# Performance work log

Measured on AMD Instinct MI355X. Metric: run time of the kernel, lower is better.

The kernel has to match this reference:

```python
import jax, jax.numpy as jnp
import numpy as np

REG_MAX = 16
BOX_W = 7.5
OBJ_W = 1.0
TOPK = 10
EPS = 1e-7


def dfl_decode(x, reg_max):
    # x: [B, 4*reg_max, N] -> expected value of per-side distribution -> [B, N, 4] (xyxy)
    B, C, N = x.shape
    x = x.reshape(B, 4, reg_max, N)
    p = jax.nn.softmax(x, axis=2)
    proj = jnp.arange(reg_max, dtype=x.dtype)
    return jnp.einsum('bkrn,r->bnk', p, proj)


def bbox_ciou(b1, b2):
    # b1: [B,N,1,4], b2: [B,1,M,4], xyxy -> [B,N,M]
    x11, y11, x12, y12 = b1[..., 0], b1[..., 1], b1[..., 2], b1[..., 3]
    x21, y21, x22, y22 = b2[..., 0], b2[..., 1], b2[..., 2], b2[..., 3]
    w1, h1 = x12 - x11, y12 - y11
    w2, h2 = x22 - x21, y22 - y21
    iw = jnp.clip(jnp.minimum(x12, x22) - jnp.maximum(x11, x21), 0.0)
    ih = jnp.clip(jnp.minimum(y12, y22) - jnp.maximum(y11, y21), 0.0)
    inter = iw * ih
    union = w1 * h1 + w2 * h2 - inter + EPS
    iou = inter / union
    cw = jnp.maximum(x12, x22) - jnp.minimum(x11, x21)
    ch = jnp.maximum(y12, y22) - jnp.minimum(y11, y21)
    c2 = cw * cw + ch * ch + EPS
    rho2 = ((x21 + x22 - x11 - x12) ** 2 + (y21 + y22 - y11 - y12) ** 2) * 0.25
    v = (4.0 / (np.pi ** 2)) * (jnp.arctan(w2 / (h2 + EPS)) - jnp.arctan(w1 / (h1 + EPS))) ** 2
    alpha = jax.lax.stop_gradient(v / (v - iou + 1.0 + EPS))
    return iou - rho2 / c2 - alpha * v


def setup_inputs() -> dict:
    key = jax.random.key(0)
    k1, k2, k3, k4 = jax.random.split(key, 4)
    B, N, M = 8, 34000, 64
    boxes = jax.random.normal(k1, (B, 4 * REG_MAX, N), dtype=jnp.float32)
    scores = jax.random.normal(k2, (B, N), dtype=jnp.float32)
    # GT boxes: valid xyxy in roughly the same [0, reg_max) range as decoded preds
    xy = jax.random.uniform(k3, (B, M, 2), dtype=jnp.float32) * 11.0
    wh = jax.random.uniform(k4, (B, M, 2), dtype=jnp.float32) * 4.0 + 0.5
    targets = jnp.concatenate([xy, xy + wh], axis=-1)
    return {'boxes': boxes, 'scores': scores, 'targets': targets}


def reference(boxes, scores, targets):
    B, N = scores.shape
    M = targets.shape[1]
    pb = dfl_decode(boxes, REG_MAX)                     # [B,N,4]
    ciou = bbox_ciou(pb[:, :, None, :], targets[:, None, :, :])  # [B,N,M]
    k = min(TOPK, N)
    topv, topi = jax.lax.top_k(jnp.swapaxes(ciou, 1, 2), k)      # [B,M,k] over anchors
    valid = topv > 0.0
    vals = jnp.where(valid, topv, 0.0)

    def per_batch(idx, val, vld):
        flat_i = idx.reshape(-1)
        iou_t = jnp.zeros((N,), val.dtype).at[flat_i].max(val.reshape(-1))
        pos = jnp.zeros((N,), bool).at[flat_i].max(vld.reshape(-1))
        return iou_t, pos

    iou_target, pos = jax.vmap(per_batch)(topi, vals, valid)     # [B,N]
    posf = pos.astype(iou_target.dtype)
    npos = posf.sum(axis=1)
    box_per = jnp.where(npos > 0,
                        ((1.0 - iou_target) * posf).sum(axis=1) / jnp.maximum(npos, 1.0),
                        0.0)
    box_loss = box_per.sum()
    # BCEWithLogits (mean over anchors), summed over batch
    bce = jnp.maximum(scores, 0.0) - scores * iou_target + jnp.log1p(jnp.exp(-jnp.abs(scores)))
    obj_loss = bce.mean(axis=1).sum()
    total = (BOX_W * box_loss + OBJ_W * obj_loss) / B
    return total, box_loss, obj_loss
```

## Files before the change

### kernel.cpp

```cpp
#include <hip/hip_runtime.h>
#include <math.h>

#define BQ 8
#define MQ 64
#define KTOP 10
#define EPSQ 1e-7f
#define APB 256
#define MBUF 1344

__device__ __forceinline__ float frcp(float x) { return __builtin_amdgcn_rcpf(x); }

#define EV16(G, OUT)                                                           \
  {                                                                            \
    float mx = fmaxf(fmaxf(fmaxf(fmaxf(G##0, G##1), fmaxf(G##2, G##3)),        \
                           fmaxf(fmaxf(G##4, G##5), fmaxf(G##6, G##7))),       \
                     fmaxf(fmaxf(fmaxf(G##8, G##9), fmaxf(G##10, G##11)),      \
                           fmaxf(fmaxf(G##12, G##13), fmaxf(G##14, G##15))));  \
    float s = 0.f, ws = 0.f, e;                                                \
    e = __expf(G##0 - mx); s += e;                                             \
    e = __expf(G##1 - mx); s += e; ws += 1.f * e;                              \
    e = __expf(G##2 - mx); s += e; ws += 2.f * e;                              \
    e = __expf(G##3 - mx); s += e; ws += 3.f * e;                              \
    e = __expf(G##4 - mx); s += e; ws += 4.f * e;                              \
    e = __expf(G##5 - mx); s += e; ws += 5.f * e;                              \
    e = __expf(G##6 - mx); s += e; ws += 6.f * e;                              \
    e = __expf(G##7 - mx); s += e; ws += 7.f * e;                              \
    e = __expf(G##8 - mx); s += e; ws += 8.f * e;                              \
    e = __expf(G##9 - mx); s += e; ws += 9.f * e;                              \
    e = __expf(G##10 - mx); s += e; ws += 10.f * e;                            \
    e = __expf(G##11 - mx); s += e; ws += 11.f * e;                            \
    e = __expf(G##12 - mx); s += e; ws += 12.f * e;                            \
    e = __expf(G##13 - mx); s += e; ws += 13.f * e;                            \
    e = __expf(G##14 - mx); s += e; ws += 14.f * e;                            \
    e = __expf(G##15 - mx); s += e; ws += 15.f * e;                            \
    OUT = ws * frcp(s);                                                        \
  }

#define DECL_LDS16(RB, G)                                                      \
  float G##0 = tile[(RB) + 0][tid], G##1 = tile[(RB) + 1][tid],                \
        G##2 = tile[(RB) + 2][tid], G##3 = tile[(RB) + 3][tid],                \
        G##4 = tile[(RB) + 4][tid], G##5 = tile[(RB) + 5][tid],                \
        G##6 = tile[(RB) + 6][tid], G##7 = tile[(RB) + 7][tid],                \
        G##8 = tile[(RB) + 8][tid], G##9 = tile[(RB) + 9][tid],                \
        G##10 = tile[(RB) + 10][tid], G##11 = tile[(RB) + 11][tid],            \
        G##12 = tile[(RB) + 12][tid], G##13 = tile[(RB) + 13][tid],            \
        G##14 = tile[(RB) + 14][tid], G##15 = tile[(RB) + 15][tid];

__global__ __launch_bounds__(256) void decode_topk_kernel(
    const float* __restrict__ boxes, const float* __restrict__ scores,
    const float* __restrict__ targets, unsigned int* __restrict__ iou_bits,
    uint2* __restrict__ cand, float* __restrict__ bcePartial,
    unsigned int* __restrict__ ctr, int N, int bpb) {
  const int tid = threadIdx.x;
  const int b = blockIdx.x / bpb;
  const int blk = blockIdx.x - b * bpb;
  const int a0 = blk * APB;
  const int w = tid >> 6;
  const int l = tid & 63;

  __shared__ __align__(16) char u_raw[32 * APB * sizeof(float)];
  float(*tile)[APB] = (float(*)[APB])u_raw;
  float* s_hv = (float*)u_raw;
  int* s_hi = (int*)(u_raw + 4 * MQ * KTOP * 4);
  uint2* s_mg = (uint2*)(u_raw + 8 * MQ * KTOP * 4);

  __shared__ float4 s_sv[APB];
  __shared__ float s_at[APB];
  __shared__ int s_ix[APB];
  __shared__ int s_cnt;
  __shared__ float s_bce;
  if (tid == 0) { s_cnt = 0; s_bce = 0.f; }
  if (blockIdx.x == 0 && tid == 0) *ctr = 0u;
  __syncthreads();

  const size_t Ns = (size_t)N;

  const int n = a0 + tid;
  float bce0 = 0.f;
  if (n < N) {
    const size_t i = (size_t)b * N + n;
    iou_bits[i] = 0u;
    float sc = scores[i];
    bce0 = fmaxf(sc, 0.f) + log1pf(__expf(-fabsf(sc)));
  }

  auto stage32 = [&](int row0) {
    const float* gbase = boxes + (size_t)(b * 64 + row0) * Ns + a0;
    if (a0 + APB <= N) {
#pragma unroll
      for (int k = 0; k < 8; ++k) {
        int idx = tid + (k << 8);
        int r = idx >> 6;
        int c = (idx & 63) << 2;
        *(float4*)&tile[r][c] = *(const float4*)(gbase + (size_t)r * Ns + c);
      }
    } else {
      int rem = N - a0;
#pragma unroll
      for (int k = 0; k < 8; ++k) {
        int idx = tid + (k << 8);
        int r = idx >> 6;
        int c = (idx & 63) << 2;
        for (int j = 0; j < 4; ++j)
          tile[r][c + j] = (c + j < rem) ? gbase[(size_t)r * Ns + c + j] : 0.f;
      }
    }
  };

  float e0, e1, e2, e3;
  stage32(0);
  __syncthreads();
  { DECL_LDS16(0, A) EV16(A, e0) }
  { DECL_LDS16(16, Bv) EV16(Bv, e1) }
  __syncthreads();
  stage32(32);
  __syncthreads();
  { DECL_LDS16(0, Cv) EV16(Cv, e2) }
  { DECL_LDS16(16, Dv) EV16(Dv, e3) }

  bool pred = false;
  float at = 0.f;
  if (n < N) {
    float w1 = e2 - e0, h1 = e3 - e1;
    if (w1 > 0.f && h1 > 0.f) {
      pred = true;
      at = atanf(w1 * frcp(h1 + EPSQ));
    }
  }
  {
    unsigned long long mask = __ballot(pred);
    int cnt = __popcll(mask);
    int bslot = 0;
    if (l == 0 && cnt) bslot = atomicAdd(&s_cnt, cnt);
    bslot = __shfl(bslot, 0, 64);
    if (pred) {
      int pos = bslot + __popcll(mask & ((1ull << l) - 1ull));
      s_sv[pos] = make_float4(e0, e1, e2, e3);
      s_at[pos] = at;
      s_ix[pos] = n;
    }
  }
#pragma unroll
  for (int d = 1; d < 64; d <<= 1) bce0 += __shfl_xor(bce0, d, 64);
  if (l == 0) atomicAdd(&s_bce, bce0);
  __syncthreads();
  const int nsurv = s_cnt;
  if (tid == 0) bcePartial[blockIdx.x] = s_bce;

  const float4 t = ((const float4*)targets)[b * MQ + l];
  const float x21 = t.x, y21 = t.y, x22 = t.z, y22 = t.w;
  const float w2 = x22 - x21, h2 = y22 - y21;
  const float atan_t = atanf(w2 * frcp(h2 + EPSQ));
  const float area2 = w2 * h2, sumx2 = x21 + x22, sumy2 = y21 + y22;
  const float CPI = 4.0f / (float)(M_PI * M_PI);

  float hv0 = 0.f, hv1 = 0.f, hv2 = 0.f, hv3 = 0.f, hv4 = 0.f;
  float hv5 = 0.f, hv6 = 0.f, hv7 = 0.f, hv8 = 0.f, hv9 = 0.f;
  int hi0 = 0, hi1 = 0, hi2 = 0, hi3 = 0, hi4 = 0;
  int hi5 = 0, hi6 = 0, hi7 = 0, hi8 = 0, hi9 = 0;

  const int qlen = (nsurv + 3) >> 2;
  const int j0 = w * qlen;
  const int j1 = min(nsurv, j0 + qlen);
  for (int j = j0; j < j1; ++j) {
    float4 p = s_sv[j];
    float pa = s_at[j];
    int ixj = s_ix[j];
    float x11 = p.x, y11 = p.y, x12 = p.z, y12 = p.w;
    float w1 = x12 - x11, h1 = y12 - y11;
    float iw = fmaxf(fminf(x12, x22) - fmaxf(x11, x21), 0.f);
    float ih = fmaxf(fminf(y12, y22) - fmaxf(y11, y21), 0.f);
    float inter = iw * ih;
    float uni = w1 * h1 + area2 - inter + EPSQ;
    float iou = inter * frcp(uni);
    float cw = fmaxf(x12, x22) - fminf(x11, x21);
    float ch = fmaxf(y12, y22) - fminf(y11, y21);
    float c2 = cw * cw + ch * ch + EPSQ;
    float dx = sumx2 - x11 - x12;
    float dy = sumy2 - y11 - y12;
    float rho2 = (dx * dx + dy * dy) * 0.25f;
    float da = atan_t - pa;
    float v = CPI * da * da;
    float alpha = v * frcp(v - iou + 1.f + EPSQ);
    float ciou = iou - rho2 * frcp(c2) - alpha * v;
    if (ciou > hv9) {
      float cv = ciou;
      int ci = ixj;
#define INS(vk, ik)                         \
  {                                         \
    bool gt = cv > vk;                      \
    float tv_ = vk; int ti_ = ik;           \
    vk = gt ? cv : vk; ik = gt ? ci : ik;   \
    cv = gt ? tv_ : cv; ci = gt ? ti_ : ci; \
  }
      INS(hv0, hi0) INS(hv1, hi1) INS(hv2, hi2) INS(hv3, hi3) INS(hv4, hi4)
      INS(hv5, hi5) INS(hv6, hi6) INS(hv7, hi7) INS(hv8, hi8) INS(hv9, hi9)
#undef INS
    }
  }
  const int hb = (w * MQ + l) * KTOP;
  s_hv[hb + 0] = hv0; s_hi[hb + 0] = hi0;
  s_hv[hb + 1] = hv1; s_hi[hb + 1] = hi1;
  s_hv[hb + 2] = hv2; s_hi[hb + 2] = hi2;
  s_hv[hb + 3] = hv3; s_hi[hb + 3] = hi3;
  s_hv[hb + 4] = hv4; s_hi[hb + 4] = hi4;
  s_hv[hb + 5] = hv5; s_hi[hb + 5] = hi5;
  s_hv[hb + 6] = hv6; s_hi[hb + 6] = hi6;
  s_hv[hb + 7] = hv7; s_hi[hb + 7] = hi7;
  s_hv[hb + 8] = hv8; s_hi[hb + 8] = hi8;
  s_hv[hb + 9] = hv9; s_hi[hb + 9] = hi9;
  __syncthreads();

  if (w == 0) {
    const int m = l;
    int p0 = 0, p1 = 0, p2 = 0, p3 = 0;
    for (int r = 0; r < KTOP; ++r) {
      float c0 = s_hv[(0 * MQ + m) * KTOP + p0];
      float c1 = s_hv[(1 * MQ + m) * KTOP + p1];
      float c2m = s_hv[(2 * MQ + m) * KTOP + p2];
      float c3 = s_hv[(3 * MQ + m) * KTOP + p3];
      float best = c0; int bw = 0;
      if (c1 > best) { best = c1; bw = 1; }
      if (c2m > best) { best = c2m; bw = 2; }
      if (c3 > best) { best = c3; bw = 3; }
      int psel = (bw == 0) ? p0 : (bw == 1) ? p1 : (bw == 2) ? p2 : p3;
      int bidx = s_hi[(bw * MQ + m) * KTOP + psel];
      s_mg[m * KTOP + r] = make_uint2(__float_as_uint(best), (unsigned)bidx);
      if (bw == 0) p0 = min(p0 + 1, KTOP - 1);
      else if (bw == 1) p1 = min(p1 + 1, KTOP - 1);
      else if (bw == 2) p2 = min(p2 + 1, KTOP - 1);
      else p3 = min(p3 + 1, KTOP - 1);
    }
  }
  __syncthreads();
  uint2* obase = cand + (size_t)(b * bpb + blk) * (MQ * KTOP);
  for (int sl = tid; sl < MQ * KTOP; sl += 256) obase[sl] = s_mg[sl];
}

__device__ __forceinline__ void select_top10(
    float* s_bv, int* s_bi, float* s_winv, int* s_wini,
    int* s_cnt, int c, int tid) {
  if (tid < 64) {
    for (int r = 0; r < KTOP; ++r) {
      float bv = 0.f;
      int bs = 0xffff;
      for (int sl = tid; sl < c; sl += 64) {
        float v = s_bv[sl];
        if (v > bv) { bv = v; bs = sl; }
      }
      unsigned long long key =
          ((unsigned long long)__float_as_uint(bv) << 32) | (unsigned int)bs;
#pragma unroll
      for (int d = 1; d < 64; d <<= 1) {
        unsigned long long o = __shfl_xor(key, d, 64);
        if (o > key) key = o;
      }
      if (tid == 0) {
        float wv = __uint_as_float((unsigned int)(key >> 32));
        int ws = (int)(key & 0xffffu);
        s_winv[r] = wv;
        if (wv > 0.f && ws != 0xffff) {
          s_wini[r] = s_bi[ws];
          s_bv[ws] = 0.f;
        } else {
          s_wini[r] = 0;
        }
      }
    }
    if (tid < KTOP) { s_bv[tid] = s_winv[tid]; s_bi[tid] = s_wini[tid]; }
    if (tid == 0) *s_cnt = KTOP;
  }
}

__global__ __launch_bounds__(256) void merge_kernel(
    const uint2* __restrict__ cand, const float* __restrict__ scores,
    unsigned int* __restrict__ iou_bits, const float* __restrict__ bcePartial,
    float* __restrict__ mergePartial, unsigned int* __restrict__ ctr,
    float* __restrict__ out, int N, int bpb) {
  const int bm = blockIdx.x;
  const int b = bm >> 6;
  const int m = bm & 63;
  const int tid = threadIdx.x;
  const int l = tid & 63;
  const int NC = bpb * KTOP;

  __shared__ float s_bv[MBUF];
  __shared__ int s_bi[MBUF];
  __shared__ float s_winv[KTOP];
  __shared__ int s_wini[KTOP];
  __shared__ int s_cnt;
  __shared__ float s_d[3];
  __shared__ int s_last;
  __shared__ float s_acc[BQ * 3];
  if (tid == 0) s_cnt = 0;
  if (tid < 3) s_d[tid] = 0.f;
  if (tid < BQ * 3) s_acc[tid] = 0.f;
  __syncthreads();

  for (int k2 = tid; k2 < NC; k2 += 256) {
    int blkk = k2 / KTOP;
    int r = k2 - blkk * KTOP;
    uint2 e = cand[((size_t)(b * bpb + blkk) * MQ + m) * KTOP + r];
    float v = __uint_as_float(e.x);
    bool p = v > 0.f;
    unsigned long long mask = __ballot(p);
    int cnt = __popcll(mask);
    int bslot = 0;
    if (l == 0 && cnt) bslot = atomicAdd(&s_cnt, cnt);
    bslot = __shfl(bslot, 0, 64);
    if (p) {
      int pos = bslot + __popcll(mask & ((1ull << l) - 1ull));
      s_bv[pos] = v;
      s_bi[pos] = (int)e.y;
    }
  }
  __syncthreads();
  int c = s_cnt;
  __syncthreads();
  if (c > KTOP) {
    select_top10(s_bv, s_bi, s_winv, s_wini, &s_cnt, c, tid);
    __syncthreads();
    c = KTOP;
  }
  if (tid < KTOP && tid < c) {
    float v = s_bv[tid];
    if (v > 0.f) {
      int ix = s_bi[tid];
      unsigned int vb = __float_as_uint(v);
      unsigned int old = atomicMax(&iou_bits[(size_t)b * N + ix], vb);
      if (old < vb) {
        float vold = __uint_as_float(old);
        bool was = (old != 0u);
        atomicAdd(&s_d[0], was ? (vold - v) : (1.f - v));
        if (!was) atomicAdd(&s_d[1], 1.f);
        atomicAdd(&s_d[2], -scores[(size_t)b * N + ix] * (v - vold));
      }
    }
  }
  __syncthreads();
  if (tid == 0) {
    float4* mp = (float4*)(mergePartial + (size_t)bm * 4);
    *mp = make_float4(s_d[0], s_d[1], s_d[2], 0.f);
    __threadfence();
    unsigned int done = atomicAdd(ctr, 1u);
    s_last = (done == (unsigned)(gridDim.x - 1)) ? 1 : 0;
  }
  __syncthreads();
  if (s_last) {
    __threadfence();
    volatile const float* mp = mergePartial;
    for (int i = tid; i < BQ * MQ; i += 256) {
      int bb = i >> 6;
      float a0 = mp[i * 4 + 0];
      float a1 = mp[i * 4 + 1];
      float a2 = mp[i * 4 + 2];
      atomicAdd(&s_acc[bb * 3 + 0], a0);
      atomicAdd(&s_acc[bb * 3 + 1], a1);
      atomicAdd(&s_acc[bb * 3 + 2], a2);
    }
    volatile const float* bp = bcePartial;
    for (int i = tid; i < BQ * bpb; i += 256) {
      int bb = i / bpb;
      atomicAdd(&s_acc[bb * 3 + 2], bp[i]);
    }
    __syncthreads();
    if (tid == 0) {
      float box = 0.f, obj = 0.f;
      for (int bb = 0; bb < BQ; ++bb) {
        float np = s_acc[bb * 3 + 1];
        box += (np > 0.f) ? s_acc[bb * 3 + 0] / fmaxf(np, 1.f) : 0.f;
        obj += s_acc[bb * 3 + 2] / (float)N;
      }
      out[0] = (7.5f * box + obj) / (float)BQ;
      out[1] = box;
      out[2] = obj;
    }
  }
}

extern "C" void kernel_launch(void* const* d_in, const int* in_sizes, int n_in,
                              void* d_out, int out_size, void* d_ws, size_t ws_size,
                              hipStream_t stream) {
  const float* boxes = (const float*)d_in[0];
  const float* scores = (const float*)d_in[1];
  const float* targets = (const float*)d_in[2];
  float* out = (float*)d_out;
  const int N = in_sizes[1] / BQ;

  const int bpb = (N + APB - 1) / APB;
  const int nblk = BQ * bpb;

  char* ws = (char*)d_ws;
  size_t cand_bytes = (size_t)BQ * bpb * MQ * KTOP * sizeof(uint2);
  size_t iou_bytes = (size_t)BQ * N * sizeof(unsigned int);
  size_t bce_bytes = (((size_t)nblk * sizeof(float)) + 255) & ~(size_t)255;
  size_t mp_bytes = (size_t)BQ * MQ * 4 * sizeof(float);

  uint2* cand = (uint2*)ws;                    ws += cand_bytes;
  unsigned int* iou_bits = (unsigned int*)ws;  ws += iou_bytes;
  float* bcePartial = (float*)ws;              ws += bce_bytes;
  float* mergePartial = (float*)ws;            ws += mp_bytes;
  unsigned int* ctr = (unsigned int*)ws;

  decode_topk_kernel<<<nblk, 256, 0, stream>>>(boxes, scores, targets,
                                               iou_bits, cand, bcePartial, ctr, N, bpb);
  merge_kernel<<<BQ * MQ, 256, 0, stream>>>(cand, scores, iou_bits, bcePartial,
                                            mergePartial, ctr, out, N, bpb);
}
```

Measured before the change: 149.2 us.

## Process two anchors per thread with 512-anchor tiles staged per side

Doubles anchors per block to 512 so each thread decodes two adjacent anchors, staging 16 DFL rows per side through a smaller LDS tile with float2 reads. Scores and iou_bits are handled in pairs. The aim is to halve block count, amortize the per-block top-k and merge work over more anchors, and raise instruction-level parallelism in the softmax. The cost is four staging rounds with extra barriers instead of two, and a larger candidate set per block for the later top-k phase. The tail path clamps loads and the hard-coded LDS offsets must still fit the shrunken union buffer.

```diff
diff --git a/kernel.cpp b/kernel.cpp
--- a/kernel.cpp
+++ b/kernel.cpp
@@ -5,46 +5,10 @@
 #define MQ 64
 #define KTOP 10
 #define EPSQ 1e-7f
-#define APB 256
+#define APB 512
 #define MBUF 1344
 
 __device__ __forceinline__ float frcp(float x) { return __builtin_amdgcn_rcpf(x); }
-
-#define EV16(G, OUT)                                                           \
-  {                                                                            \
-    float mx = fmaxf(fmaxf(fmaxf(fmaxf(G##0, G##1), fmaxf(G##2, G##3)),        \
-                           fmaxf(fmaxf(G##4, G##5), fmaxf(G##6, G##7))),       \
-                     fmaxf(fmaxf(fmaxf(G##8, G##9), fmaxf(G##10, G##11)),      \
-                           fmaxf(fmaxf(G##12, G##13), fmaxf(G##14, G##15))));  \
-    float s = 0.f, ws = 0.f, e;                                                \
-    e = __expf(G##0 - mx); s += e;                                             \
-    e = __expf(G##1 - mx); s += e; ws += 1.f * e;                              \
-    e = __expf(G##2 - mx); s += e; ws += 2.f * e;                              \
-    e = __expf(G##3 - mx); s += e; ws += 3.f * e;                              \
-    e = __expf(G##4 - mx); s += e; ws += 4.f * e;                              \
-    e = __expf(G##5 - mx); s += e; ws += 5.f * e;                              \
-    e = __expf(G##6 - mx); s += e; ws += 6.f * e;                              \
-    e = __expf(G##7 - mx); s += e; ws += 7.f * e;                              \
-    e = __expf(G##8 - mx); s += e; ws += 8.f * e;                              \
-    e = __expf(G##9 - mx); s += e; ws += 9.f * e;                              \
-    e = __expf(G##10 - mx); s += e; ws += 10.f * e;                            \
-    e = __expf(G##11 - mx); s += e; ws += 11.f * e;                            \
-    e = __expf(G##12 - mx); s += e; ws += 12.f * e;                            \
-    e = __expf(G##13 - mx); s += e; ws += 13.f * e;                            \
-    e = __expf(G##14 - mx); s += e; ws += 14.f * e;                            \
-    e = __expf(G##15 - mx); s += e; ws += 15.f * e;                            \
-    OUT = ws * frcp(s);                                                        \
-  }
-
-#define DECL_LDS16(RB, G)                                                      \
-  float G##0 = tile[(RB) + 0][tid], G##1 = tile[(RB) + 1][tid],                \
-        G##2 = tile[(RB) + 2][tid], G##3 = tile[(RB) + 3][tid],                \
-        G##4 = tile[(RB) + 4][tid], G##5 = tile[(RB) + 5][tid],                \
-        G##6 = tile[(RB) + 6][tid], G##7 = tile[(RB) + 7][tid],                \
-        G##8 = tile[(RB) + 8][tid], G##9 = tile[(RB) + 9][tid],                \
-        G##10 = tile[(RB) + 10][tid], G##11 = tile[(RB) + 11][tid],            \
-        G##12 = tile[(RB) + 12][tid], G##13 = tile[(RB) + 13][tid],            \
-        G##14 = tile[(RB) + 14][tid], G##15 = tile[(RB) + 15][tid];
 
 __global__ __launch_bounds__(256) void decode_topk_kernel(
     const float* __restrict__ boxes, const float* __restrict__ scores,
@@ -58,12 +22,11 @@
   const int w = tid >> 6;
   const int l = tid & 63;
 
-  __shared__ __align__(16) char u_raw[32 * APB * sizeof(float)];
+  __shared__ __align__(16) char u_raw[16 * APB * sizeof(float)];
   float(*tile)[APB] = (float(*)[APB])u_raw;
   float* s_hv = (float*)u_raw;
-  int* s_hi = (int*)(u_raw + 4 * MQ * KTOP * 4);
-  uint2* s_mg = (uint2*)(u_raw + 8 * MQ * KTOP * 4);
-
+  int* s_hi = (int*)(u_raw + 10240);
+  uint2* s_mg = (uint2*)(u_raw + 20480);
   __shared__ float4 s_sv[APB];
   __shared__ float s_at[APB];
   __shared__ int s_ix[APB];
@@ -74,70 +37,125 @@
   __syncthreads();
 
   const size_t Ns = (size_t)N;
-
-  const int n = a0 + tid;
+  const int n0 = a0 + 2 * tid;
+  const bool tail = (a0 + APB > N);
+
   float bce0 = 0.f;
-  if (n < N) {
-    const size_t i = (size_t)b * N + n;
-    iou_bits[i] = 0u;
-    float sc = scores[i];
-    bce0 = fmaxf(sc, 0.f) + log1pf(__expf(-fabsf(sc)));
-  }
-
-  auto stage32 = [&](int row0) {
-    const float* gbase = boxes + (size_t)(b * 64 + row0) * Ns + a0;
-    if (a0 + APB <= N) {
+  if (n0 < N) {
+    const size_t i = (size_t)b * N + n0;
+    if (n0 + 1 < N && ((i & 1) == 0)) {
+      iou_bits[i] = 0u; iou_bits[i + 1] = 0u;
+      float2 sc = *(const float2*)(scores + i);
+      bce0 = fmaxf(sc.x, 0.f) + log1pf(__expf(-fabsf(sc.x))) +
+             fmaxf(sc.y, 0.f) + log1pf(__expf(-fabsf(sc.y)));
+    } else if (n0 + 1 < N) {
+      iou_bits[i] = 0u; iou_bits[i + 1] = 0u;
+      float sa = scores[i], sb = scores[i + 1];
+      bce0 = fmaxf(sa, 0.f) + log1pf(__expf(-fabsf(sa))) +
+             fmaxf(sb, 0.f) + log1pf(__expf(-fabsf(sb)));
+    } else {
+      iou_bits[i] = 0u;
+      float sc = scores[i];
+      bce0 = fmaxf(sc, 0.f) + log1pf(__expf(-fabsf(sc)));
+    }
+  }
+
+  const int tcol = 2 * tid;
+  float ev_a[4], ev_b[4];
+#pragma unroll
+  for (int s = 0; s < 4; ++s) {
+    const float* gside = boxes + (size_t)(b * 64 + s * 16) * Ns;
+    if (!tail) {
 #pragma unroll
       for (int k = 0; k < 8; ++k) {
         int idx = tid + (k << 8);
-        int r = idx >> 6;
-        int c = (idx & 63) << 2;
-        *(float4*)&tile[r][c] = *(const float4*)(gbase + (size_t)r * Ns + c);
+        int r = idx >> 7;
+        int c = (idx & 127) << 2;
+        *(float4*)&tile[r][c] = *(const float4*)(gside + (size_t)r * Ns + a0 + c);
       }
     } else {
-      int rem = N - a0;
 #pragma unroll
       for (int k = 0; k < 8; ++k) {
         int idx = tid + (k << 8);
-        int r = idx >> 6;
-        int c = (idx & 63) << 2;
-        for (int j = 0; j < 4; ++j)
-          tile[r][c + j] = (c + j < rem) ? gbase[(size_t)r * Ns + c + j] : 0.f;
-      }
-    }
-  };
-
-  float e0, e1, e2, e3;
-  stage32(0);
-  __syncthreads();
-  { DECL_LDS16(0, A) EV16(A, e0) }
-  { DECL_LDS16(16, Bv) EV16(Bv, e1) }
-  __syncthreads();
-  stage32(32);
-  __syncthreads();
-  { DECL_LDS16(0, Cv) EV16(Cv, e2) }
-  { DECL_LDS16(16, Dv) EV16(Dv, e3) }
-
-  bool pred = false;
-  float at = 0.f;
-  if (n < N) {
-    float w1 = e2 - e0, h1 = e3 - e1;
-    if (w1 > 0.f && h1 > 0.f) {
-      pred = true;
-      at = atanf(w1 * frcp(h1 + EPSQ));
-    }
-  }
+        int r = idx >> 7;
+        int c = (idx & 127) << 2;
+        int gc = a0 + c;
+        if (gc > N - 4) gc = N - 4;
+        if (gc < 0) gc = 0;
+        *(float4*)&tile[r][c] = *(const float4*)(gside + (size_t)r * Ns + gc);
+      }
+    }
+    __syncthreads();
+    float2 x0 = *(const float2*)&tile[0][tcol];
+    float2 x1 = *(const float2*)&tile[1][tcol];
+    float2 x2 = *(const float2*)&tile[2][tcol];
+    float2 x3 = *(const float2*)&tile[3][tcol];
+    float2 x4 = *(const float2*)&tile[4][tcol];
+    float2 x5 = *(const float2*)&tile[5][tcol];
+    float2 x6 = *(const float2*)&tile[6][tcol];
+    float2 x7 = *(const float2*)&tile[7][tcol];
+    float2 x8 = *(const float2*)&tile[8][tcol];
+    float2 x9 = *(const float2*)&tile[9][tcol];
+    float2 x10 = *(const float2*)&tile[10][tcol];
+    float2 x11 = *(const float2*)&tile[11][tcol];
+    float2 x12 = *(const float2*)&tile[12][tcol];
+    float2 x13 = *(const float2*)&tile[13][tcol];
+    float2 x14 = *(const float2*)&tile[14][tcol];
+    float2 x15 = *(const float2*)&tile[15][tcol];
+    float mxa = fmaxf(fmaxf(fmaxf(fmaxf(x0.x, x1.x), fmaxf(x2.x, x3.x)),
+                            fmaxf(fmaxf(x4.x, x5.x), fmaxf(x6.x, x7.x))),
+                      fmaxf(fmaxf(fmaxf(x8.x, x9.x), fmaxf(x10.x, x11.x)),
+                            fmaxf(fmaxf(x12.x, x13.x), fmaxf(x14.x, x15.x))));
+    float mxb = fmaxf(fmaxf(fmaxf(fmaxf(x0.y, x1.y), fmaxf(x2.y, x3.y)),
+                            fmaxf(fmaxf(x4.y, x5.y), fmaxf(x6.y, x7.y))),
+                      fmaxf(fmaxf(fmaxf(x8.y, x9.y), fmaxf(x10.y, x11.y)),
+                            fmaxf(fmaxf(x12.y, x13.y), fmaxf(x14.y, x15.y))));
+    float sa = 0.f, wa = 0.f, sb = 0.f, wb = 0.f, e;
+#define STEP(K, XK)                                    \
+    e = __expf(XK.x - mxa); sa += e; wa += (float)K * e; \
+    e = __expf(XK.y - mxb); sb += e; wb += (float)K * e;
+    STEP(0, x0) STEP(1, x1) STEP(2, x2) STEP(3, x3)
+    STEP(4, x4) STEP(5, x5) STEP(6, x6) STEP(7, x7)
+    STEP(8, x8) STEP(9, x9) STEP(10, x10) STEP(11, x11)
+    STEP(12, x12) STEP(13, x13) STEP(14, x14) STEP(15, x15)
+#undef STEP
+    ev_a[s] = wa * frcp(sa);
+    ev_b[s] = wb * frcp(sb);
+    __syncthreads();
+  }
+
   {
-    unsigned long long mask = __ballot(pred);
-    int cnt = __popcll(mask);
-    int bslot = 0;
-    if (l == 0 && cnt) bslot = atomicAdd(&s_cnt, cnt);
-    bslot = __shfl(bslot, 0, 64);
-    if (pred) {
-      int pos = bslot + __popcll(mask & ((1ull << l) - 1ull));
-      s_sv[pos] = make_float4(e0, e1, e2, e3);
-      s_at[pos] = at;
-      s_ix[pos] = n;
+    bool pa = false, pb = false;
+    float ata = 0.f, atb = 0.f;
+    if (n0 < N) {
+      float w1 = ev_a[2] - ev_a[0], h1 = ev_a[3] - ev_a[1];
+      if (w1 > 0.f && h1 > 0.f) { pa = true; ata = atanf(w1 * frcp(h1 + EPSQ)); }
+    }
+    if (n0 + 1 < N) {
+      float w1 = ev_b[2] - ev_b[0], h1 = ev_b[3] - ev_b[1];
+      if (w1 > 0.f && h1 > 0.f) { pb = true; atb = atanf(w1 * frcp(h1 + EPSQ)); }
+    }
+    unsigned long long ma = __ballot(pa);
+    int ca = __popcll(ma);
+    int sa_ = 0;
+    if (l == 0 && ca) sa_ = atomicAdd(&s_cnt, ca);
+    sa_ = __shfl(sa_, 0, 64);
+    if (pa) {
+      int pos = sa_ + __popcll(ma & ((1ull << l) - 1ull));
+      s_sv[pos] = make_float4(ev_a[0], ev_a[1], ev_a[2], ev_a[3]);
+      s_at[pos] = ata;
+      s_ix[pos] = n0;
+    }
+    unsigned long long mb = __ballot(pb);
+    int cb = __popcll(mb);
+    int sb_ = 0;
+    if (l == 0 && cb) sb_ = atomicAdd(&s_cnt, cb);
+    sb_ = __shfl(sb_, 0, 64);
+    if (pb) {
+      int pos = sb_ + __popcll(mb & ((1ull << l) - 1ull));
+      s_sv[pos] = make_float4(ev_b[0], ev_b[1], ev_b[2], ev_b[3]);
+      s_at[pos] = atb;
+      s_ix[pos] = n0 + 1;
     }
   }
 #pragma unroll
```

After: 140.5 us. 5.9% less time.
